# Kernel tuning notes

Measured on AMD Instinct MI355X. Metric: run time of the kernel, lower is better.

## Reference

```python
import jax, jax.numpy as jnp
import numpy as np

B, T, C, H = 4, 2048, 1024, 16
HD = C // H  # head_size = 64
EPS = 1e-5


def setup_inputs() -> dict:
    key = jax.random.key(0)
    ks = jax.random.split(key, 16)
    s_c = 1.0 / np.sqrt(C)
    s_4c = 1.0 / np.sqrt(4 * C)
    return {
        "x": jax.random.normal(ks[0], (B, T, C), jnp.float32),
        # per-head projections, stored [H, C, HD] (already in x@W orientation)
        "wq": jax.random.uniform(ks[1], (H, C, HD), jnp.float32, -s_c, s_c),
        "wk": jax.random.uniform(ks[2], (H, C, HD), jnp.float32, -s_c, s_c),
        "wv": jax.random.uniform(ks[3], (H, C, HD), jnp.float32, -s_c, s_c),
        "w_proj": jax.random.uniform(ks[4], (C, C), jnp.float32, -s_c, s_c),
        "b_proj": jax.random.uniform(ks[5], (C,), jnp.float32, -s_c, s_c),
        "w1": jax.random.uniform(ks[6], (C, 4 * C), jnp.float32, -s_c, s_c),
        "b1": jax.random.uniform(ks[7], (4 * C,), jnp.float32, -s_c, s_c),
        "w2": jax.random.uniform(ks[8], (4 * C, C), jnp.float32, -s_4c, s_4c),
        "b2": jax.random.uniform(ks[9], (C,), jnp.float32, -s_4c, s_4c),
        "ln1_g": jnp.ones((C,), jnp.float32),
        "ln1_b": jnp.zeros((C,), jnp.float32),
        "ln2_g": jnp.ones((C,), jnp.float32),
        "ln2_b": jnp.zeros((C,), jnp.float32),
    }


def layer_norm(x, g, b):
    mu = jnp.mean(x, axis=-1, keepdims=True)
    var = jnp.mean(jnp.square(x - mu), axis=-1, keepdims=True)
    return (x - mu) * jax.lax.rsqrt(var + EPS) * g + b


def reference(x, wq, wk, wv, w_proj, b_proj, w1, b1, w2, b2, ln1_g, ln1_b, ln2_g, ln2_b):
    Bc, Tc, Cc = x.shape
    h = layer_norm(x, ln1_g, ln1_b)
    q = jnp.einsum("btc,hcd->bhtd", h, wq)
    k = jnp.einsum("btc,hcd->bhtd", h, wk)
    v = jnp.einsum("btc,hcd->bhtd", h, wv)
    scale = HD ** -0.5
    wei = jnp.einsum("bhtd,bhsd->bhts", q, k) * scale  # [B,H,T,T]
    causal = jnp.tril(jnp.ones((Tc, Tc), bool))
    wei = jnp.where(causal, wei, -jnp.inf)
    wei = jax.nn.softmax(wei, axis=-1)
    att = jnp.einsum("bhts,bhsd->bhtd", wei, v)
    att = att.transpose(0, 2, 1, 3).reshape(Bc, Tc, Cc)  # concat heads
    x = x + att @ w_proj + b_proj
    h2 = layer_norm(x, ln2_g, ln2_b)
    ff = jax.nn.relu(h2 @ w1 + b1) @ w2 + b2
    return x + ff
```

## Files before the change

kernel.cpp:

```cpp
#include <hip/hip_runtime.h>


#define B_ 4
#define T_ 2048
#define C_ 1024
#define H_ 16
#define BT_ 8192

typedef __attribute__((ext_vector_type(8))) __bf16 bf16x8;
typedef __attribute__((ext_vector_type(4))) __bf16 bf16x4;
typedef __attribute__((ext_vector_type(4))) float f32x4;

#define WAIT_LGKM0 asm volatile("s_waitcnt lgkmcnt(0)" ::: "memory")
#define WAIT_VM(N) asm volatile("s_waitcnt vmcnt(" #N ")" ::: "memory")

__device__ __forceinline__ void gload_lds16(const void* g, void* l) {
  __builtin_amdgcn_global_load_lds((const __attribute__((address_space(1))) void*)g,
                                   (__attribute__((address_space(3))) void*)l, 16, 0, 0);
}

__device__ __forceinline__ void block_sync() {
  asm volatile("" ::: "memory");
  __builtin_amdgcn_s_barrier();
  asm volatile("" ::: "memory");
}

__global__ __launch_bounds__(256) void transpose_f32_bf16(
    const float* __restrict__ in, __bf16* __restrict__ out,
    int R, int Cc, long inBatch, long outBatch) {
  __shared__ float tile[32][33];
  const int tx = threadIdx.x, ty = threadIdx.y;
  in += (long)blockIdx.z * inBatch;
  out += (long)blockIdx.z * outBatch;
  const int r0 = blockIdx.y * 32, c0 = blockIdx.x * 32;
#pragma unroll
  for (int i = 0; i < 4; i++)
    tile[ty + i * 8][tx] = in[(long)(r0 + ty + i * 8) * Cc + c0 + tx];
  __syncthreads();
#pragma unroll
  for (int i = 0; i < 4; i++)
    out[(long)(c0 + ty + i * 8) * R + r0 + tx] = (__bf16)tile[tx][ty + i * 8];
}

__global__ __launch_bounds__(256) void ln_fwd(const float* __restrict__ x,
                                              const float* __restrict__ g,
                                              const float* __restrict__ bta,
                                              __bf16* __restrict__ out) {
  const long row = blockIdx.x;
  const int tid = threadIdx.x;
  float4 v = ((const float4*)(x + row * C_))[tid];
  float vals[4] = {v.x, v.y, v.z, v.w};
  float s = vals[0] + vals[1] + vals[2] + vals[3];
  float s2 = vals[0] * vals[0] + vals[1] * vals[1] + vals[2] * vals[2] + vals[3] * vals[3];
#pragma unroll
  for (int o = 1; o < 64; o <<= 1) {
    s += __shfl_xor(s, o);
    s2 += __shfl_xor(s2, o);
  }
  __shared__ float red[8];
  const int lane = tid & 63, wid = tid >> 6;
  if (lane == 0) { red[wid] = s; red[wid + 4] = s2; }
  __syncthreads();
  const float S = red[0] + red[1] + red[2] + red[3];
  const float S2 = red[4] + red[5] + red[6] + red[7];
  const float mu = S * (1.0f / C_);
  const float var = S2 * (1.0f / C_) - mu * mu;
  const float rs = rsqrtf(var + 1e-5f);
  bf16x4 o4;
#pragma unroll
  for (int j = 0; j < 4; j++) {
    const int c = tid * 4 + j;
    o4[j] = (__bf16)((vals[j] - mu) * rs * g[c] + bta[c]);
  }
  *(bf16x4*)(out + row * C_ + tid * 4) = o4;
}

template <int EPI>
__global__ __launch_bounds__(512, 2) void gemm8p(
    const __bf16* __restrict__ A, const __bf16* __restrict__ Bt,
    void* out0, void* out1, void* out2,
    const float* __restrict__ bias, const float* __restrict__ resid,
    int M, int N, int K, int nwg) {
  __shared__ __bf16 sm[49152];
  __bf16* ldsA = &sm[0];
  __bf16* ldsB = &sm[16384];
  const int tid = threadIdx.x, lane = tid & 63, wid = tid >> 6;
  const int wm = wid >> 2, wn = wid & 3;
  const int l15 = lane & 15, qtr = lane >> 4;
  const int q8 = nwg >> 3;
  const int wg = (blockIdx.x & 7) * q8 + (blockIdx.x >> 3);
  const int mBlocks = M >> 7;
  const long mBase = (long)(wg % mBlocks) * 128;
  const long nBase = (long)(wg / mBlocks) * 256;
  const int NT = K >> 6;

  f32x4 acc[4][4] = {};

  const int spos = (tid & 3) ^ ((tid >> 3) & 3);
  const __bf16* aS = A + (mBase + (tid >> 2)) * (long)K + spos * 8;
  const __bf16* bS0 = Bt + (nBase + (tid >> 2)) * (long)K + spos * 8;
  const __bf16* bS1 = bS0 + 128 * (long)K;

  const int posRd = (qtr ^ ((l15 >> 1) & 3)) * 8;
  const int aRd = (wm * 64 + l15) * 32 + posRd;
  const int bRd = (wn * 64 + l15) * 32 + posRd;

#define STG_A(BUF, KT, KH) gload_lds16(aS + (KT) * 64 + (KH) * 32, ldsA + (BUF) * 8192 + (KH) * 4096 + tid * 8)
#define STG_B(BUF, KT, KH)                                                                    \
  do {                                                                                        \
    gload_lds16(bS0 + (KT) * 64 + (KH) * 32, ldsB + (BUF) * 16384 + (KH) * 8192 + tid * 8);   \
    gload_lds16(bS1 + (KT) * 64 + (KH) * 32, ldsB + (BUF) * 16384 + (KH) * 8192 + 4096 + tid * 8); \
  } while (0)

#define GPHASE(BUF, KH, VMN, ...)                                                          \
  do {                                                                                     \
    bf16x8 af0 = *(const bf16x8*)&ldsA[(BUF) * 8192 + (KH) * 4096 + aRd];                  \
    bf16x8 af1 = *(const bf16x8*)&ldsA[(BUF) * 8192 + (KH) * 4096 + aRd + 512];            \
    bf16x8 af2 = *(const bf16x8*)&ldsA[(BUF) * 8192 + (KH) * 4096 + aRd + 1024];           \
    bf16x8 af3 = *(const bf16x8*)&ldsA[(BUF) * 8192 + (KH) * 4096 + aRd + 1536];           \
    bf16x8 bf0 = *(const bf16x8*)&ldsB[(BUF) * 16384 + (KH) * 8192 + bRd];                 \
    bf16x8 bf1 = *(const bf16x8*)&ldsB[(BUF) * 16384 + (KH) * 8192 + bRd + 512];           \
    bf16x8 bf2 = *(const bf16x8*)&ldsB[(BUF) * 16384 + (KH) * 8192 + bRd + 1024];          \
    bf16x8 bf3 = *(const bf16x8*)&ldsB[(BUF) * 16384 + (KH) * 8192 + bRd + 1536];          \
    __VA_ARGS__;                                                                           \
    WAIT_VM(VMN);                                                                          \
    block_sync();                                                                          \
    WAIT_LGKM0;                                                                            \
    __builtin_amdgcn_sched_barrier(0);                                                     \
    __builtin_amdgcn_s_setprio(1);                                                         \
    acc[0][0] = __builtin_amdgcn_mfma_f32_16x16x32_bf16(af0, bf0, acc[0][0], 0, 0, 0);     \
    acc[0][1] = __builtin_amdgcn_mfma_f32_16x16x32_bf16(af0, bf1, acc[0][1], 0, 0, 0);     \
    acc[0][2] = __builtin_amdgcn_mfma_f32_16x16x32_bf16(af0, bf2, acc[0][2], 0, 0, 0);     \
    acc[0][3] = __builtin_amdgcn_mfma_f32_16x16x32_bf16(af0, bf3, acc[0][3], 0, 0, 0);     \
    acc[1][0] = __builtin_amdgcn_mfma_f32_16x16x32_bf16(af1, bf0, acc[1][0], 0, 0, 0);     \
    acc[1][1] = __builtin_amdgcn_mfma_f32_16x16x32_bf16(af1, bf1, acc[1][1], 0, 0, 0);     \
    acc[1][2] = __builtin_amdgcn_mfma_f32_16x16x32_bf16(af1, bf2, acc[1][2], 0, 0, 0);     \
    acc[1][3] = __builtin_amdgcn_mfma_f32_16x16x32_bf16(af1, bf3, acc[1][3], 0, 0, 0);     \
    acc[2][0] = __builtin_amdgcn_mfma_f32_16x16x32_bf16(af2, bf0, acc[2][0], 0, 0, 0);     \
    acc[2][1] = __builtin_amdgcn_mfma_f32_16x16x32_bf16(af2, bf1, acc[2][1], 0, 0, 0);     \
    acc[2][2] = __builtin_amdgcn_mfma_f32_16x16x32_bf16(af2, bf2, acc[2][2], 0, 0, 0);     \
    acc[2][3] = __builtin_amdgcn_mfma_f32_16x16x32_bf16(af2, bf3, acc[2][3], 0, 0, 0);     \
    acc[3][0] = __builtin_amdgcn_mfma_f32_16x16x32_bf16(af3, bf0, acc[3][0], 0, 0, 0);     \
    acc[3][1] = __builtin_amdgcn_mfma_f32_16x16x32_bf16(af3, bf1, acc[3][1], 0, 0, 0);     \
    acc[3][2] = __builtin_amdgcn_mfma_f32_16x16x32_bf16(af3, bf2, acc[3][2], 0, 0, 0);     \
    acc[3][3] = __builtin_amdgcn_mfma_f32_16x16x32_bf16(af3, bf3, acc[3][3], 0, 0, 0);     \
    __builtin_amdgcn_s_setprio(0);                                                         \
    block_sync();                                                                          \
  } while (0)

  STG_A(0, 0, 0); STG_B(0, 0, 0);
  STG_A(0, 0, 1); STG_B(0, 0, 1);
  STG_A(1, 1, 0); STG_B(1, 1, 0);
  WAIT_VM(6);
  block_sync();

  for (int T = 0; T + 3 < NT; T += 2) {
    GPHASE(0, 0, 6, STG_A(1, T + 1, 1); STG_B(1, T + 1, 1));
    GPHASE(0, 1, 6, STG_A(0, T + 2, 0); STG_B(0, T + 2, 0));
    GPHASE(1, 0, 6, STG_A(0, T + 2, 1); STG_B(0, T + 2, 1));
    GPHASE(1, 1, 6, STG_A(1, T + 3, 0); STG_B(1, T + 3, 0));
  }
  GPHASE(0, 0, 6, STG_A(1, NT - 1, 1); STG_B(1, NT - 1, 1));
  GPHASE(0, 1, 3, );
  GPHASE(1, 0, 0, );
  GPHASE(1, 1, 0, );

#undef GPHASE
#undef STG_A
#undef STG_B

  if (EPI == 0) {
    __bf16* outB = (__bf16*)out0;
#pragma unroll
    for (int cf = 0; cf < 4; cf++) {
      const long gc = nBase + wn * 64 + cf * 16 + l15;
      const float bv = bias[gc];
#pragma unroll
      for (int rf = 0; rf < 4; rf++) {
        const long gr0 = mBase + wm * 64 + rf * 16 + qtr * 4;
#pragma unroll
        for (int r = 0; r < 4; r++)
          outB[(gr0 + r) * (long)N + gc] = (__bf16)fmaxf(acc[rf][cf][r] + bv, 0.0f);
      }
    }
  } else if (EPI == 2) {
    float* outF = (float*)out0;
#pragma unroll
    for (int cf = 0; cf < 4; cf++) {
      const long gc = nBase + wn * 64 + cf * 16 + l15;
      const float bv = bias[gc];
#pragma unroll
      for (int rf = 0; rf < 4; rf++) {
        const long gr0 = mBase + wm * 64 + rf * 16 + qtr * 4;
#pragma unroll
        for (int r = 0; r < 4; r++)
          outF[(gr0 + r) * (long)N + gc] = acc[rf][cf][r] + bv + resid[(gr0 + r) * (long)N + gc];
      }
    }
  } else {
    const int seg = (int)(nBase >> 10);
#pragma unroll
    for (int cf = 0; cf < 4; cf++) {
      const long gc = nBase + wn * 64 + cf * 16 + l15;
      const long cc = gc & 1023;
#pragma unroll
      for (int rf = 0; rf < 4; rf++) {
        const long gr0 = mBase + wm * 64 + rf * 16 + qtr * 4;
        if (seg == 0) {
          __bf16* Qb = (__bf16*)out0;
#pragma unroll
          for (int r = 0; r < 4; r++) Qb[(gr0 + r) * 1024 + cc] = (__bf16)acc[rf][cf][r];
        } else if (seg == 1) {
          __bf16* Kb = (__bf16*)out1;
#pragma unroll
          for (int r = 0; r < 4; r++) Kb[(gr0 + r) * 1024 + cc] = (__bf16)acc[rf][cf][r];
        } else {
          __bf16* Vtg = (__bf16*)out2;
          bf16x4 v4;
#pragma unroll
          for (int r = 0; r < 4; r++) v4[r] = (__bf16)acc[rf][cf][r];
          *(bf16x4*)&Vtg[cc * (long)BT_ + gr0] = v4;
        }
      }
    }
  }
}

#define PSTR 72
__global__ __launch_bounds__(512, 6) void attn_fwd2(
    const __bf16* __restrict__ Qg, const __bf16* __restrict__ Kg,
    const __bf16* __restrict__ Vtg, __bf16* __restrict__ O) {
  __shared__ __bf16 Ks[2][64 * 64];
  __shared__ __bf16 Vs[2][64 * 64];
  __shared__ __bf16 Ps[128 * PSTR];
  const int tid = threadIdx.x, lane = tid & 63, wid = tid >> 6;
  const int bh = blockIdx.x, b = bh >> 4, h = bh & 15;
  const int qx = 15 - blockIdx.y;
  const int qBase = qx * 128;
  const int qw = qBase + wid * 16;
  const int qwTop = qw + 15;
  const long bT = (long)b * T_;
  const int l15 = lane & 15, qtr = lane >> 4;
  const int q_lane = qw + l15;

  const int srow = tid >> 3;
  const int schunk = (tid & 7) ^ (srow & 7);
  const __bf16* kSrcBase = Kg + (bT + srow) * C_ + h * 64 + schunk * 8;
  const __bf16* vSrcBase = Vtg + (long)(h * 64 + srow) * BT_ + bT + schunk * 8;
  __bf16* kDst = &Ks[0][tid * 8];
  __bf16* vDst = &Vs[0][tid * 8];
  const int bufStride = 64 * 64;

  bf16x8 q0s, q1s;
  {
    const float SC = 0.125f * 1.44269504089f;
    bf16x8 r0 = *(const bf16x8*)(Qg + (bT + q_lane) * C_ + h * 64 + qtr * 8);
    bf16x8 r1 = *(const bf16x8*)(Qg + (bT + q_lane) * C_ + h * 64 + 32 + qtr * 8);
#pragma unroll
    for (int j = 0; j < 8; j++) {
      q0s[j] = (__bf16)((float)r0[j] * SC);
      q1s[j] = (__bf16)((float)r1[j] * SC);
    }
  }

  f32x4 o[4] = {};
  float m_ = -1e30f, l_ = 0.0f;
  const int nkt = 2 * qx + 2;

  gload_lds16(kSrcBase, kDst);
  gload_lds16(vSrcBase, vDst);
  __syncthreads();

  int buf = 0;
  for (int t = 0; t < nkt; t++) {
    const int k0 = t * 64;
    if (t + 1 < nkt) {
      const long koff = (long)(k0 + 64);
      gload_lds16(kSrcBase + koff * C_, kDst + (buf ^ 1) * bufStride);
      gload_lds16(vSrcBase + koff, vDst + (buf ^ 1) * bufStride);
    }
    if (k0 <= qwTop) {
      const __bf16* ks = Ks[buf];
      const __bf16* vs = Vs[buf];
      f32x4 sT[4] = {};
      __builtin_amdgcn_s_setprio(1);
#pragma unroll
      for (int kb = 0; kb < 4; kb++) {
        bf16x8 aK0 = *(const bf16x8*)&ks[(kb * 16 + l15) * 64 + ((qtr ^ (l15 & 7)) * 8)];
        bf16x8 aK1 = *(const bf16x8*)&ks[(kb * 16 + l15) * 64 + (((4 + qtr) ^ (l15 & 7)) * 8)];
        sT[kb] = __builtin_amdgcn_mfma_f32_16x16x32_bf16(aK0, q0s, sT[kb], 0, 0, 0);
        sT[kb] = __builtin_amdgcn_mfma_f32_16x16x32_bf16(aK1, q1s, sT[kb], 0, 0, 0);
      }
      __builtin_amdgcn_s_setprio(0);
      if (k0 + 63 > qw) {
#pragma unroll
        for (int kb = 0; kb < 4; kb++)
#pragma unroll
          for (int r = 0; r < 4; r++)
            if (k0 + kb * 16 + qtr * 4 + r > q_lane) sT[kb][r] = -1e30f;
      }
      float mx = -1e30f;
#pragma unroll
      for (int kb = 0; kb < 4; kb++)
#pragma unroll
        for (int r = 0; r < 4; r++) mx = fmaxf(mx, sT[kb][r]);
      mx = fmaxf(mx, __shfl_xor(mx, 16));
      mx = fmaxf(mx, __shfl_xor(mx, 32));
      const bool defer = __all(mx - m_ <= 8.0f);
      const float mnew = defer ? m_ : fmaxf(m_, mx);
      float psum = 0.0f;
#pragma unroll
      for (int kb = 0; kb < 4; kb++)
#pragma unroll
        for (int r = 0; r < 4; r++) {
          const float pv = exp2f(sT[kb][r] - mnew);
          psum += pv;
          Ps[(wid * 16 + l15) * PSTR + kb * 16 + qtr * 4 + r] = (__bf16)pv;
        }
      psum += __shfl_xor(psum, 16);
      psum += __shfl_xor(psum, 32);
      if (defer) {
        l_ += psum;
      } else {
        const float fac = exp2f(m_ - mnew);
        l_ = l_ * fac + psum;
        m_ = mnew;
#pragma unroll
        for (int r = 0; r < 4; r++) {
          const float fr = __shfl(fac, (lane & 48) + qtr * 4 + r);
#pragma unroll
          for (int dg = 0; dg < 4; dg++) o[dg][r] *= fr;
        }
      }
      __builtin_amdgcn_s_setprio(1);
#pragma unroll
      for (int s = 0; s < 2; s++) {
        bf16x8 aP = *(const bf16x8*)&Ps[(wid * 16 + l15) * PSTR + s * 32 + qtr * 8];
#pragma unroll
        for (int dg = 0; dg < 4; dg++) {
          bf16x8 bV = *(const bf16x8*)&vs[(dg * 16 + l15) * 64 + (((s * 4 + qtr) ^ (l15 & 7)) * 8)];
          o[dg] = __builtin_amdgcn_mfma_f32_16x16x32_bf16(aP, bV, o[dg], 0, 0, 0);
        }
      }
      __builtin_amdgcn_s_setprio(0);
    }
    __syncthreads();
    buf ^= 1;
  }

  const float linv = 1.0f / l_;
#pragma unroll
  for (int r = 0; r < 4; r++) {
    const float lr = __shfl(linv, (lane & 48) + qtr * 4 + r);
    const long row = bT + qw + qtr * 4 + r;
#pragma unroll
    for (int dg = 0; dg < 4; dg++)
      O[row * C_ + h * 64 + dg * 16 + l15] = (__bf16)(o[dg][r] * lr);
  }
}

extern "C" void kernel_launch(void* const* d_in, const int* in_sizes, int n_in,
                              void* d_out, int out_size, void* d_ws, size_t ws_size,
                              hipStream_t stream) {
  const float* x = (const float*)d_in[0];
  const float* wq = (const float*)d_in[1];
  const float* wk = (const float*)d_in[2];
  const float* wv = (const float*)d_in[3];
  const float* wproj = (const float*)d_in[4];
  const float* bproj = (const float*)d_in[5];
  const float* w1 = (const float*)d_in[6];
  const float* b1 = (const float*)d_in[7];
  const float* w2 = (const float*)d_in[8];
  const float* b2 = (const float*)d_in[9];
  const float* g1 = (const float*)d_in[10];
  const float* be1 = (const float*)d_in[11];
  const float* g2 = (const float*)d_in[12];
  const float* be2 = (const float*)d_in[13];

  char* ws = (char*)d_ws;
  const size_t MB = 1024ull * 1024ull;
  __bf16* h1 = (__bf16*)(ws + 0);
  __bf16* Qb = (__bf16*)(ws + 16 * MB);
  __bf16* Kb = (__bf16*)(ws + 32 * MB);
  __bf16* Vtg = (__bf16*)(ws + 48 * MB);
  __bf16* ff1 = (__bf16*)(ws + 32 * MB);
  __bf16* wqt = (__bf16*)(ws + 96 * MB);
  __bf16* wkt = (__bf16*)(ws + 98 * MB);
  __bf16* wvt = (__bf16*)(ws + 100 * MB);
  __bf16* wpt = (__bf16*)(ws + 102 * MB);
  __bf16* w1t = (__bf16*)(ws + 104 * MB);
  __bf16* w2t = (__bf16*)(ws + 112 * MB);
  __bf16* att = h1;
  __bf16* h2 = Qb;
  float* xout = (float*)d_out;

  dim3 tb(32, 8);
  transpose_f32_bf16<<<dim3(2, 32, 16), tb, 0, stream>>>(wq, wqt, 1024, 64, 1024 * 64, 64 * 1024);
  transpose_f32_bf16<<<dim3(2, 32, 16), tb, 0, stream>>>(wk, wkt, 1024, 64, 1024 * 64, 64 * 1024);
  transpose_f32_bf16<<<dim3(2, 32, 16), tb, 0, stream>>>(wv, wvt, 1024, 64, 1024 * 64, 64 * 1024);
  transpose_f32_bf16<<<dim3(32, 32, 1), tb, 0, stream>>>(wproj, wpt, 1024, 1024, 0, 0);
  transpose_f32_bf16<<<dim3(128, 32, 1), tb, 0, stream>>>(w1, w1t, 1024, 4096, 0, 0);
  transpose_f32_bf16<<<dim3(32, 128, 1), tb, 0, stream>>>(w2, w2t, 4096, 1024, 0, 0);

  ln_fwd<<<8192, 256, 0, stream>>>(x, g1, be1, h1);
  gemm8p<1><<<768, 512, 0, stream>>>(h1, wqt, Qb, Kb, Vtg, nullptr, nullptr, 8192, 3072, 1024, 768);
  attn_fwd2<<<dim3(64, 16), 512, 0, stream>>>(Qb, Kb, Vtg, att);
  gemm8p<2><<<256, 512, 0, stream>>>(att, wpt, xout, nullptr, nullptr, bproj, x, 8192, 1024, 1024, 256);
  ln_fwd<<<8192, 256, 0, stream>>>(xout, g2, be2, h2);
  gemm8p<0><<<1024, 512, 0, stream>>>(h2, w1t, ff1, nullptr, nullptr, b1, nullptr, 8192, 4096, 1024, 1024);
  gemm8p<2><<<256, 512, 0, stream>>>(ff1, w2t, xout, nullptr, nullptr, b2, (const float*)xout, 8192, 1024, 4096, 256);
}
```

Before: 383.8 us.

## Use 256x256 GEMM tiles with B-fragment reuse and split-K atomics for FF2

The GEMM tile grows from 128x256 to 256x256 per workgroup, with each wave covering 128 rows. B fragments are loaded once per K-half and reused across two A row-halves, raising arithmetic intensity per LDS read. The final FF2 GEMM uses a 2-way split-K whose partial sums are added with atomics onto the residual already in the output, so it keeps enough workgroups. In exchange, LDS grows to 128KB per block, which likely caps occupancy at one block per CU. The projection GEMM now launches only 128 workgroups, and the atomic accumulation order is nondeterministic.

Result: slower. 436.6 us (+13.8%).

```diff
diff --git a/kernel.cpp b/kernel.cpp
--- a/kernel.cpp
+++ b/kernel.cpp
@@ -13,6 +13,7 @@
 
 #define WAIT_LGKM0 asm volatile("s_waitcnt lgkmcnt(0)" ::: "memory")
 #define WAIT_VM(N) asm volatile("s_waitcnt vmcnt(" #N ")" ::: "memory")
+#define NOSTG ((void)0)
 
 __device__ __forceinline__ void gload_lds16(const void* g, void* l) {
   __builtin_amdgcn_global_load_lds((const __attribute__((address_space(1))) void*)g,
@@ -75,99 +76,117 @@
   *(bf16x4*)(out + row * C_ + tid * 4) = o4;
 }
 
-template <int EPI>
-__global__ __launch_bounds__(512, 2) void gemm8p(
+template <int EPI, int SPLITK>
+__global__ __launch_bounds__(512, 2) void gemm2x(
     const __bf16* __restrict__ A, const __bf16* __restrict__ Bt,
     void* out0, void* out1, void* out2,
     const float* __restrict__ bias, const float* __restrict__ resid,
     int M, int N, int K, int nwg) {
-  __shared__ __bf16 sm[49152];
+  __shared__ __bf16 sm[65536];
   __bf16* ldsA = &sm[0];
-  __bf16* ldsB = &sm[16384];
+  __bf16* ldsB = &sm[32768];
   const int tid = threadIdx.x, lane = tid & 63, wid = tid >> 6;
   const int wm = wid >> 2, wn = wid & 3;
   const int l15 = lane & 15, qtr = lane >> 4;
   const int q8 = nwg >> 3;
-  const int wg = (blockIdx.x & 7) * q8 + (blockIdx.x >> 3);
-  const int mBlocks = M >> 7;
-  const long mBase = (long)(wg % mBlocks) * 128;
+  int wg = (blockIdx.x & 7) * q8 + (blockIdx.x >> 3);
+  int k0 = 0, KS = K;
+  if (SPLITK) { KS = K >> 1; k0 = (wg >> 7) * KS; wg &= 127; }
+  const int mBlocks = M >> 8;
+  const long mBase = (long)(wg % mBlocks) * 256;
   const long nBase = (long)(wg / mBlocks) * 256;
-  const int NT = K >> 6;
-
-  f32x4 acc[4][4] = {};
+  const int NT = KS >> 6;
+
+  f32x4 acc[8][4] = {};
+  bf16x8 bfr[4];
+
+  const int posRd = (qtr ^ ((l15 >> 1) & 3)) * 8;
+  const int aRdB = (wm * 128 + l15) * 32 + posRd;
+  const int bRdB = (wn * 64 + l15) * 32 + posRd;
 
   const int spos = (tid & 3) ^ ((tid >> 3) & 3);
-  const __bf16* aS = A + (mBase + (tid >> 2)) * (long)K + spos * 8;
-  const __bf16* bS0 = Bt + (nBase + (tid >> 2)) * (long)K + spos * 8;
+  const __bf16* aS0 = A + (mBase + (tid >> 2)) * (long)K + k0 + spos * 8;
+  const __bf16* aS1 = aS0 + 128 * (long)K;
+  const __bf16* bS0 = Bt + (nBase + (tid >> 2)) * (long)K + k0 + spos * 8;
   const __bf16* bS1 = bS0 + 128 * (long)K;
 
-  const int posRd = (qtr ^ ((l15 >> 1) & 3)) * 8;
-  const int aRd = (wm * 64 + l15) * 32 + posRd;
-  const int bRd = (wn * 64 + l15) * 32 + posRd;
-
-#define STG_A(BUF, KT, KH) gload_lds16(aS + (KT) * 64 + (KH) * 32, ldsA + (BUF) * 8192 + (KH) * 4096 + tid * 8)
-#define STG_B(BUF, KT, KH)                                                                    \
+#define STGA(BUF, KH, KT)                                                                     \
   do {                                                                                        \
-    gload_lds16(bS0 + (KT) * 64 + (KH) * 32, ldsB + (BUF) * 16384 + (KH) * 8192 + tid * 8);   \
-    gload_lds16(bS1 + (KT) * 64 + (KH) * 32, ldsB + (BUF) * 16384 + (KH) * 8192 + 4096 + tid * 8); \
+    gload_lds16(aS0 + (KT) * 64 + (KH) * 32, ldsA + ((BUF) * 2 + (KH)) * 8192 + tid * 8);     \
+    gload_lds16(aS1 + (KT) * 64 + (KH) * 32, ldsA + ((BUF) * 2 + (KH)) * 8192 + 4096 + tid * 8); \
   } while (0)
-
-#define GPHASE(BUF, KH, VMN, ...)                                                          \
-  do {                                                                                     \
-    bf16x8 af0 = *(const bf16x8*)&ldsA[(BUF) * 8192 + (KH) * 4096 + aRd];                  \
-    bf16x8 af1 = *(const bf16x8*)&ldsA[(BUF) * 8192 + (KH) * 4096 + aRd + 512];            \
-    bf16x8 af2 = *(const bf16x8*)&ldsA[(BUF) * 8192 + (KH) * 4096 + aRd + 1024];           \
-    bf16x8 af3 = *(const bf16x8*)&ldsA[(BUF) * 8192 + (KH) * 4096 + aRd + 1536];           \
-    bf16x8 bf0 = *(const bf16x8*)&ldsB[(BUF) * 16384 + (KH) * 8192 + bRd];                 \
-    bf16x8 bf1 = *(const bf16x8*)&ldsB[(BUF) * 16384 + (KH) * 8192 + bRd + 512];           \
-    bf16x8 bf2 = *(const bf16x8*)&ldsB[(BUF) * 16384 + (KH) * 8192 + bRd + 1024];          \
-    bf16x8 bf3 = *(const bf16x8*)&ldsB[(BUF) * 16384 + (KH) * 8192 + bRd + 1536];          \
-    __VA_ARGS__;                                                                           \
-    WAIT_VM(VMN);                                                                          \
-    block_sync();                                                                          \
-    WAIT_LGKM0;                                                                            \
-    __builtin_amdgcn_sched_barrier(0);                                                     \
-    __builtin_amdgcn_s_setprio(1);                                                         \
-    acc[0][0] = __builtin_amdgcn_mfma_f32_16x16x32_bf16(af0, bf0, acc[0][0], 0, 0, 0);     \
-    acc[0][1] = __builtin_amdgcn_mfma_f32_16x16x32_bf16(af0, bf1, acc[0][1], 0, 0, 0);     \
-    acc[0][2] = __builtin_amdgcn_mfma_f32_16x16x32_bf16(af0, bf2, acc[0][2], 0, 0, 0);     \
-    acc[0][3] = __builtin_amdgcn_mfma_f32_16x16x32_bf16(af0, bf3, acc[0][3], 0, 0, 0);     \
-    acc[1][0] = __builtin_amdgcn_mfma_f32_16x16x32_bf16(af1, bf0, acc[1][0], 0, 0, 0);     \
-    acc[1][1] = __builtin_amdgcn_mfma_f32_16x16x32_bf16(af1, bf1, acc[1][1], 0, 0, 0);     \
-    acc[1][2] = __builtin_amdgcn_mfma_f32_16x16x32_bf16(af1, bf2, acc[1][2], 0, 0, 0);     \
-    acc[1][3] = __builtin_amdgcn_mfma_f32_16x16x32_bf16(af1, bf3, acc[1][3], 0, 0, 0);     \
-    acc[2][0] = __builtin_amdgcn_mfma_f32_16x16x32_bf16(af2, bf0, acc[2][0], 0, 0, 0);     \
-    acc[2][1] = __builtin_amdgcn_mfma_f32_16x16x32_bf16(af2, bf1, acc[2][1], 0, 0, 0);     \
-    acc[2][2] = __builtin_amdgcn_mfma_f32_16x16x32_bf16(af2, bf2, acc[2][2], 0, 0, 0);     \
-    acc[2][3] = __builtin_amdgcn_mfma_f32_16x16x32_bf16(af2, bf3, acc[2][3], 0, 0, 0);     \
-    acc[3][0] = __builtin_amdgcn_mfma_f32_16x16x32_bf16(af3, bf0, acc[3][0], 0, 0, 0);     \
-    acc[3][1] = __builtin_amdgcn_mfma_f32_16x16x32_bf16(af3, bf1, acc[3][1], 0, 0, 0);     \
-    acc[3][2] = __builtin_amdgcn_mfma_f32_16x16x32_bf16(af3, bf2, acc[3][2], 0, 0, 0);     \
-    acc[3][3] = __builtin_amdgcn_mfma_f32_16x16x32_bf16(af3, bf3, acc[3][3], 0, 0, 0);     \
-    __builtin_amdgcn_s_setprio(0);                                                         \
-    block_sync();                                                                          \
+#define STGB(BUF, KH, KT)                                                                     \
+  do {                                                                                        \
+    gload_lds16(bS0 + (KT) * 64 + (KH) * 32, ldsB + ((BUF) * 2 + (KH)) * 8192 + tid * 8);     \
+    gload_lds16(bS1 + (KT) * 64 + (KH) * 32, ldsB + ((BUF) * 2 + (KH)) * 8192 + 4096 + tid * 8); \
   } while (0)
 
-  STG_A(0, 0, 0); STG_B(0, 0, 0);
-  STG_A(0, 0, 1); STG_B(0, 0, 1);
-  STG_A(1, 1, 0); STG_B(1, 1, 0);
-  WAIT_VM(6);
+#define PH(BUF, KH, RFH, WAITOP, STG)                                                        \
+  do {                                                                                       \
+    const __bf16* sA_ = ldsA + ((BUF) * 2 + (KH)) * 8192;                                    \
+    const __bf16* sB_ = ldsB + ((BUF) * 2 + (KH)) * 8192;                                    \
+    bf16x8 af0 = *(const bf16x8*)&sA_[aRdB + (RFH) * 2048];                                  \
+    bf16x8 af1 = *(const bf16x8*)&sA_[aRdB + (RFH) * 2048 + 512];                            \
+    bf16x8 af2 = *(const bf16x8*)&sA_[aRdB + (RFH) * 2048 + 1024];                           \
+    bf16x8 af3 = *(const bf16x8*)&sA_[aRdB + (RFH) * 2048 + 1536];                           \
+    if ((RFH) == 0) {                                                                        \
+      bfr[0] = *(const bf16x8*)&sB_[bRdB];                                                   \
+      bfr[1] = *(const bf16x8*)&sB_[bRdB + 512];                                             \
+      bfr[2] = *(const bf16x8*)&sB_[bRdB + 1024];                                            \
+      bfr[3] = *(const bf16x8*)&sB_[bRdB + 1536];                                            \
+    }                                                                                        \
+    STG;                                                                                     \
+    WAITOP;                                                                                  \
+    block_sync();                                                                            \
+    WAIT_LGKM0;                                                                              \
+    __builtin_amdgcn_sched_barrier(0);                                                       \
+    __builtin_amdgcn_s_setprio(1);                                                           \
+    acc[(RFH)*4+0][0] = __builtin_amdgcn_mfma_f32_16x16x32_bf16(af0, bfr[0], acc[(RFH)*4+0][0], 0, 0, 0); \
+    acc[(RFH)*4+0][1] = __builtin_amdgcn_mfma_f32_16x16x32_bf16(af0, bfr[1], acc[(RFH)*4+0][1], 0, 0, 0); \
+    acc[(RFH)*4+0][2] = __builtin_amdgcn_mfma_f32_16x16x32_bf16(af0, bfr[2], acc[(RFH)*4+0][2], 0, 0, 0); \
+    acc[(RFH)*4+0][3] = __builtin_amdgcn_mfma_f32_16x16x32_bf16(af0, bfr[3], acc[(RFH)*4+0][3], 0, 0, 0); \
+    acc[(RFH)*4+1][0] = __builtin_amdgcn_mfma_f32_16x16x32_bf16(af1, bfr[0], acc[(RFH)*4+1][0], 0, 0, 0); \
+    acc[(RFH)*4+1][1] = __builtin_amdgcn_mfma_f32_16x16x32_bf16(af1, bfr[1], acc[(RFH)*4+1][1], 0, 0, 0); \
+    acc[(RFH)*4+1][2] = __builtin_amdgcn_mfma_f32_16x16x32_bf16(af1, bfr[2], acc[(RFH)*4+1][2], 0, 0, 0); \
+    acc[(RFH)*4+1][3] = __builtin_amdgcn_mfma_f32_16x16x32_bf16(af1, bfr[3], acc[(RFH)*4+1][3], 0, 0, 0); \
+    acc[(RFH)*4+2][0] = __builtin_amdgcn_mfma_f32_16x16x32_bf16(af2, bfr[0], acc[(RFH)*4+2][0], 0, 0, 0); \
+    acc[(RFH)*4+2][1] = __builtin_amdgcn_mfma_f32_16x16x32_bf16(af2, bfr[1], acc[(RFH)*4+2][1], 0, 0, 0); \
+    acc[(RFH)*4+2][2] = __builtin_amdgcn_mfma_f32_16x16x32_bf16(af2, bfr[2], acc[(RFH)*4+2][2], 0, 0, 0); \
+    acc[(RFH)*4+2][3] = __builtin_amdgcn_mfma_f32_16x16x32_bf16(af2, bfr[3], acc[(RFH)*4+2][3], 0, 0, 0); \
+    acc[(RFH)*4+3][0] = __builtin_amdgcn_mfma_f32_16x16x32_bf16(af3, bfr[0], acc[(RFH)*4+3][0], 0, 0, 0); \
+    acc[(RFH)*4+3][1] = __builtin_amdgcn_mfma_f32_16x16x32_bf16(af3, bfr[1], acc[(RFH)*4+3][1], 0, 0, 0); \
+    acc[(RFH)*4+3][2] = __builtin_amdgcn_mfma_f32_16x16x32_bf16(af3, bfr[2], acc[(RFH)*4+3][2], 0, 0, 0); \
+    acc[(RFH)*4+3][3] = __builtin_amdgcn_mfma_f32_16x16x32_bf16(af3, bfr[3], acc[(RFH)*4+3][3], 0, 0, 0); \
+    __builtin_amdgcn_s_setprio(0);                                                           \
+    block_sync();                                                                            \
+  } while (0)
+
+  STGA(0, 0, 0); STGB(0, 0, 0);
+  STGA(0, 1, 0); STGB(0, 1, 0);
+  STGA(1, 0, 1); STGB(1, 0, 1);
+  WAIT_VM(8);
   block_sync();
 
-  for (int T = 0; T + 3 < NT; T += 2) {
-    GPHASE(0, 0, 6, STG_A(1, T + 1, 1); STG_B(1, T + 1, 1));
-    GPHASE(0, 1, 6, STG_A(0, T + 2, 0); STG_B(0, T + 2, 0));
-    GPHASE(1, 0, 6, STG_A(0, T + 2, 1); STG_B(0, T + 2, 1));
-    GPHASE(1, 1, 6, STG_A(1, T + 3, 0); STG_B(1, T + 3, 0));
-  }
-  GPHASE(0, 0, 6, STG_A(1, NT - 1, 1); STG_B(1, NT - 1, 1));
-  GPHASE(0, 1, 3, );
-  GPHASE(1, 0, 0, );
-  GPHASE(1, 1, 0, );
-
-#undef GPHASE
-#undef STG_A
-#undef STG_B
+  int b = 0;
+  for (int t = 0; t + 2 < NT; ++t) {
+    PH(b, 0, 0, NOSTG, STGA(b ^ 1, 1, t + 1));
+    PH(b, 0, 1, WAIT_VM(8), STGB(b ^ 1, 1, t + 1));
+    PH(b, 1, 0, NOSTG, STGA(b, 0, t + 2));
+    PH(b, 1, 1, WAIT_VM(8), STGB(b, 0, t + 2));
+    b ^= 1;
+  }
+  PH(0, 0, 0, NOSTG, STGA(1, 1, NT - 1));
+  PH(0, 0, 1, WAIT_VM(8), STGB(1, 1, NT - 1));
+  PH(0, 1, 0, NOSTG, NOSTG);
+  PH(0, 1, 1, WAIT_VM(4), NOSTG);
+  PH(1, 0, 0, NOSTG, NOSTG);
+  PH(1, 0, 1, WAIT_VM(0), NOSTG);
+  PH(1, 1, 0, NOSTG, NOSTG);
+  PH(1, 1, 1, WAIT_VM(0), NOSTG);
+
+#undef PH
+#undef STGA
+#undef STGB
 
   if (EPI == 0) {
     __bf16* outB = (__bf16*)out0;
@@ -176,8 +195,8 @@
       const long gc = nBase + wn * 64 + cf * 16 + l15;
       const float bv = bias[gc];
 #pragma unroll
-      for (int rf = 0; rf < 4; rf++) {
-        const long gr0 = mBase + wm * 64 + rf * 16 + qtr * 4;
+      for (int rf = 0; rf < 8; rf++) {
+        const long gr0 = mBase + wm * 128 + rf * 16 + qtr * 4;
 #pragma unroll
         for (int r = 0; r < 4; r++)
           outB[(gr0 + r) * (long)N + gc] = (__bf16)fmaxf(acc[rf][cf][r] + bv, 0.0f);
@@ -190,11 +209,25 @@
       const long gc = nBase + wn * 64 + cf * 16 + l15;
       const float bv = bias[gc];
 #pragma unroll
-      for (int rf = 0; rf < 4; rf++) {
-        const long gr0 = mBase + wm * 64 + rf * 16 + qtr * 4;
+      for (int rf = 0; rf < 8; rf++) {
+        const long gr0 = mBase + wm * 128 + rf * 16 + qtr * 4;
 #pragma unroll
         for (int r = 0; r < 4; r++)
           outF[(gr0 + r) * (long)N + gc] = acc[rf][cf][r] + bv + resid[(gr0 + r) * (long)N + gc];
+      }
+    }
+  } else if (EPI == 3) {
+    float* outF = (float*)out0;
+#pragma unroll
+    for (int cf = 0; cf < 4; cf++) {
+      const long gc = nBase + wn * 64 + cf * 16 + l15;
+      const float bv = (k0 == 0) ? bias[gc] : 0.0f;
+#pragma unroll
+      for (int rf = 0; rf < 8; rf++) {
+        const long gr0 = mBase + wm * 128 + rf * 16 + qtr * 4;
+#pragma unroll
+        for (int r = 0; r < 4; r++)
+          atomicAdd(&outF[(gr0 + r) * (long)N + gc], acc[rf][cf][r] + bv);
       }
     }
   } else {
@@ -204,8 +237,8 @@
       const long gc = nBase + wn * 64 + cf * 16 + l15;
       const long cc = gc & 1023;
 #pragma unroll
-      for (int rf = 0; rf < 4; rf++) {
-        const long gr0 = mBase + wm * 64 + rf * 16 + qtr * 4;
+      for (int rf = 0; rf < 8; rf++) {
+        const long gr0 = mBase + wm * 128 + rf * 16 + qtr * 4;
         if (seg == 0) {
           __bf16* Qb = (__bf16*)out0;
 #pragma unroll
@@ -403,10 +436,10 @@
   transpose_f32_bf16<<<dim3(32, 128, 1), tb, 0, stream>>>(w2, w2t, 4096, 1024, 0, 0);
 
   ln_fwd<<<8192, 256, 0, stream>>>(x, g1, be1, h1);
-  gemm8p<1><<<768, 512, 0, stream>>>(h1, wqt, Qb, Kb, Vtg, nullptr, nullptr, 8192, 3072, 1024, 768);
+  gemm2x<1, 0><<<384, 512, 0, stream>>>(h1, wqt, Qb, Kb, Vtg, nullptr, nullptr, 8192, 3072, 1024, 384);
   attn_fwd2<<<dim3(64, 16), 512, 0, stream>>>(Qb, Kb, Vtg, att);
-  gemm8p<2><<<256, 512, 0, stream>>>(att, wpt, xout, nullptr, nullptr, bproj, x, 8192, 1024, 1024, 256);
+  gemm2x<2, 0><<<128, 512, 0, stream>>>(att, wpt, xout, nullptr, nullptr, bproj, x, 8192, 1024, 1024, 128);
   ln_fwd<<<8192, 256, 0, stream>>>(xout, g2, be2, h2);
-  gemm8p<0><<<1024, 512, 0, stream>>>(h2, w1t, ff1, nullptr, nullptr, b1, nullptr, 8192, 4096, 1024, 1024);
-  gemm8p<2><<<256, 512, 0, stream>>>(ff1, w2t, xout, nullptr, nullptr, b2, (const float*)xout, 8192, 1024, 4096, 256);
-}
+  gemm2x<0, 0><<<512, 512, 0, stream>>>(h2, w1t, ff1, nullptr, nullptr, b1, nullptr, 8192, 4096, 1024, 512);
+  gemm2x<3, 1><<<256, 512, 0, stream>>>(ff1, w2t, xout, nullptr, nullptr, b2, nullptr, 8192, 1024, 4096, 256);
+}
```

## Process 32 query rows per wave in attention to reuse K/V tiles

Applied to the files above, without the earlier changes.

The attention kernel now gives each wave two 16-row query sub-tiles (256 queries per block, 8 blocks per head instead of 16). Each K and V fragment read from LDS therefore feeds twice as many MFMAs, and the per-block K/V global loads are amortized over more queries. P tiles are written to LDS as packed 4-element vectors instead of scalars. The cost is more registers (launch bounds lowered from 6 to 4 waves/SIMD), a larger P buffer, fewer blocks for load balance, and more wasted work on causal-diagonal tiles.

Measured after the change: 393.2 us. 2.4% more time.

```diff
diff --git a/kernel.cpp b/kernel.cpp
--- a/kernel.cpp
+++ b/kernel.cpp
@@ -227,21 +227,19 @@
 }
 
 #define PSTR 72
-__global__ __launch_bounds__(512, 6) void attn_fwd2(
+__global__ __launch_bounds__(512, 4) void attn_fwd3(
     const __bf16* __restrict__ Qg, const __bf16* __restrict__ Kg,
     const __bf16* __restrict__ Vtg, __bf16* __restrict__ O) {
   __shared__ __bf16 Ks[2][64 * 64];
   __shared__ __bf16 Vs[2][64 * 64];
-  __shared__ __bf16 Ps[128 * PSTR];
+  __shared__ __bf16 Ps[256 * PSTR];
   const int tid = threadIdx.x, lane = tid & 63, wid = tid >> 6;
   const int bh = blockIdx.x, b = bh >> 4, h = bh & 15;
-  const int qx = 15 - blockIdx.y;
-  const int qBase = qx * 128;
-  const int qw = qBase + wid * 16;
-  const int qwTop = qw + 15;
+  const int qx = 7 - blockIdx.y;
+  const int qB = qx * 256;
+  const int qw = qB + wid * 32;
   const long bT = (long)b * T_;
   const int l15 = lane & 15, qtr = lane >> 4;
-  const int q_lane = qw + l15;
 
   const int srow = tid >> 3;
   const int schunk = (tid & 7) ^ (srow & 7);
@@ -251,21 +249,29 @@
   __bf16* vDst = &Vs[0][tid * 8];
   const int bufStride = 64 * 64;
 
-  bf16x8 q0s, q1s;
+  __bf16* psW0 = &Ps[(wid * 32 + l15) * PSTR + qtr * 4];
+  __bf16* psW1 = psW0 + 16 * PSTR;
+  const __bf16* psR0 = &Ps[(wid * 32 + l15) * PSTR + qtr * 8];
+  const __bf16* psR1 = psR0 + 16 * PSTR;
+
+  bf16x8 q0s[2], q1s[2];
   {
     const float SC = 0.125f * 1.44269504089f;
-    bf16x8 r0 = *(const bf16x8*)(Qg + (bT + q_lane) * C_ + h * 64 + qtr * 8);
-    bf16x8 r1 = *(const bf16x8*)(Qg + (bT + q_lane) * C_ + h * 64 + 32 + qtr * 8);
-#pragma unroll
-    for (int j = 0; j < 8; j++) {
-      q0s[j] = (__bf16)((float)r0[j] * SC);
-      q1s[j] = (__bf16)((float)r1[j] * SC);
-    }
-  }
-
-  f32x4 o[4] = {};
-  float m_ = -1e30f, l_ = 0.0f;
-  const int nkt = 2 * qx + 2;
+#pragma unroll
+    for (int hf = 0; hf < 2; hf++) {
+      bf16x8 r0 = *(const bf16x8*)(Qg + (bT + qw + l15) * C_ + h * 64 + hf * 32 + qtr * 8);
+      bf16x8 r1 = *(const bf16x8*)(Qg + (bT + qw + 16 + l15) * C_ + h * 64 + hf * 32 + qtr * 8);
+#pragma unroll
+      for (int j = 0; j < 8; j++) {
+        q0s[hf][j] = (__bf16)((float)r0[j] * SC);
+        q1s[hf][j] = (__bf16)((float)r1[j] * SC);
+      }
+    }
+  }
+
+  f32x4 o0[4] = {}, o1[4] = {};
+  float m0 = -1e30f, m1 = -1e30f, l0 = 0.0f, l1 = 0.0f;
+  const int nkt = 4 * qx + 4;
 
   gload_lds16(kSrcBase, kDst);
   gload_lds16(vSrcBase, vDst);
@@ -279,67 +285,86 @@
       gload_lds16(kSrcBase + koff * C_, kDst + (buf ^ 1) * bufStride);
       gload_lds16(vSrcBase + koff, vDst + (buf ^ 1) * bufStride);
     }
-    if (k0 <= qwTop) {
+    if (k0 <= qw + 31) {
       const __bf16* ks = Ks[buf];
       const __bf16* vs = Vs[buf];
-      f32x4 sT[4] = {};
+      f32x4 sT0[4] = {}, sT1[4] = {};
       __builtin_amdgcn_s_setprio(1);
 #pragma unroll
       for (int kb = 0; kb < 4; kb++) {
         bf16x8 aK0 = *(const bf16x8*)&ks[(kb * 16 + l15) * 64 + ((qtr ^ (l15 & 7)) * 8)];
         bf16x8 aK1 = *(const bf16x8*)&ks[(kb * 16 + l15) * 64 + (((4 + qtr) ^ (l15 & 7)) * 8)];
-        sT[kb] = __builtin_amdgcn_mfma_f32_16x16x32_bf16(aK0, q0s, sT[kb], 0, 0, 0);
-        sT[kb] = __builtin_amdgcn_mfma_f32_16x16x32_bf16(aK1, q1s, sT[kb], 0, 0, 0);
+        sT0[kb] = __builtin_amdgcn_mfma_f32_16x16x32_bf16(aK0, q0s[0], sT0[kb], 0, 0, 0);
+        sT0[kb] = __builtin_amdgcn_mfma_f32_16x16x32_bf16(aK1, q0s[1], sT0[kb], 0, 0, 0);
+        sT1[kb] = __builtin_amdgcn_mfma_f32_16x16x32_bf16(aK0, q1s[0], sT1[kb], 0, 0, 0);
+        sT1[kb] = __builtin_amdgcn_mfma_f32_16x16x32_bf16(aK1, q1s[1], sT1[kb], 0, 0, 0);
       }
       __builtin_amdgcn_s_setprio(0);
       if (k0 + 63 > qw) {
 #pragma unroll
         for (int kb = 0; kb < 4; kb++)
 #pragma unroll
-          for (int r = 0; r < 4; r++)
-            if (k0 + kb * 16 + qtr * 4 + r > q_lane) sT[kb][r] = -1e30f;
-      }
-      float mx = -1e30f;
+          for (int r = 0; r < 4; r++) {
+            const int kk = k0 + kb * 16 + qtr * 4 + r;
+            if (kk > qw + l15) sT0[kb][r] = -1e30f;
+            if (kk > qw + 16 + l15) sT1[kb][r] = -1e30f;
+          }
+      }
+      float mx0 = -1e30f, mx1 = -1e30f;
 #pragma unroll
       for (int kb = 0; kb < 4; kb++)
 #pragma unroll
-        for (int r = 0; r < 4; r++) mx = fmaxf(mx, sT[kb][r]);
-      mx = fmaxf(mx, __shfl_xor(mx, 16));
-      mx = fmaxf(mx, __shfl_xor(mx, 32));
-      const bool defer = __all(mx - m_ <= 8.0f);
-      const float mnew = defer ? m_ : fmaxf(m_, mx);
-      float psum = 0.0f;
-#pragma unroll
-      for (int kb = 0; kb < 4; kb++)
-#pragma unroll
         for (int r = 0; r < 4; r++) {
-          const float pv = exp2f(sT[kb][r] - mnew);
-          psum += pv;
-          Ps[(wid * 16 + l15) * PSTR + kb * 16 + qtr * 4 + r] = (__bf16)pv;
+          mx0 = fmaxf(mx0, sT0[kb][r]);
+          mx1 = fmaxf(mx1, sT1[kb][r]);
         }
-      psum += __shfl_xor(psum, 16);
-      psum += __shfl_xor(psum, 32);
+      mx0 = fmaxf(mx0, __shfl_xor(mx0, 16));
+      mx0 = fmaxf(mx0, __shfl_xor(mx0, 32));
+      mx1 = fmaxf(mx1, __shfl_xor(mx1, 16));
+      mx1 = fmaxf(mx1, __shfl_xor(mx1, 32));
+      const bool defer = __all(mx0 - m0 <= 8.0f && mx1 - m1 <= 8.0f);
+      const float mn0 = defer ? m0 : fmaxf(m0, mx0);
+      const float mn1 = defer ? m1 : fmaxf(m1, mx1);
+      float ps0 = 0.0f, ps1 = 0.0f;
+#pragma unroll
+      for (int kb = 0; kb < 4; kb++) {
+        bf16x4 p4a, p4b;
+#pragma unroll
+        for (int r = 0; r < 4; r++) {
+          const float pa = exp2f(sT0[kb][r] - mn0);
+          const float pb = exp2f(sT1[kb][r] - mn1);
+          ps0 += pa; ps1 += pb;
+          p4a[r] = (__bf16)pa; p4b[r] = (__bf16)pb;
+        }
+        *(bf16x4*)&psW0[kb * 16] = p4a;
+        *(bf16x4*)&psW1[kb * 16] = p4b;
+      }
+      ps0 += __shfl_xor(ps0, 16); ps0 += __shfl_xor(ps0, 32);
+      ps1 += __shfl_xor(ps1, 16); ps1 += __shfl_xor(ps1, 32);
       if (defer) {
-        l_ += psum;
+        l0 += ps0; l1 += ps1;
       } else {
-        const float fac = exp2f(m_ - mnew);
-        l_ = l_ * fac + psum;
-        m_ = mnew;
+        const float f0 = exp2f(m0 - mn0), f1 = exp2f(m1 - mn1);
+        l0 = l0 * f0 + ps0; l1 = l1 * f1 + ps1;
+        m0 = mn0; m1 = mn1;
 #pragma unroll
         for (int r = 0; r < 4; r++) {
-          const float fr = __shfl(fac, (lane & 48) + qtr * 4 + r);
-#pragma unroll
-          for (int dg = 0; dg < 4; dg++) o[dg][r] *= fr;
+          const float fr0 = __shfl(f0, (lane & 48) + qtr * 4 + r);
+          const float fr1 = __shfl(f1, (lane & 48) + qtr * 4 + r);
+#pragma unroll
+          for (int dg = 0; dg < 4; dg++) { o0[dg][r] *= fr0; o1[dg][r] *= fr1; }
         }
       }
       __builtin_amdgcn_s_setprio(1);
 #pragma unroll
       for (int s = 0; s < 2; s++) {
-        bf16x8 aP = *(const bf16x8*)&Ps[(wid * 16 + l15) * PSTR + s * 32 + qtr * 8];
+        bf16x8 aP0 = *(const bf16x8*)&psR0[s * 32];
+        bf16x8 aP1 = *(const bf16x8*)&psR1[s * 32];
 #pragma unroll
         for (int dg = 0; dg < 4; dg++) {
           bf16x8 bV = *(const bf16x8*)&vs[(dg * 16 + l15) * 64 + (((s * 4 + qtr) ^ (l15 & 7)) * 8)];
-          o[dg] = __builtin_amdgcn_mfma_f32_16x16x32_bf16(aP, bV, o[dg], 0, 0, 0);
+          o0[dg] = __builtin_amdgcn_mfma_f32_16x16x32_bf16(aP0, bV, o0[dg], 0, 0, 0);
+          o1[dg] = __builtin_amdgcn_mfma_f32_16x16x32_bf16(aP1, bV, o1[dg], 0, 0, 0);
         }
       }
       __builtin_amdgcn_s_setprio(0);
@@ -348,14 +373,17 @@
     buf ^= 1;
   }
 
-  const float linv = 1.0f / l_;
+  const float li0 = 1.0f / l0, li1 = 1.0f / l1;
 #pragma unroll
   for (int r = 0; r < 4; r++) {
-    const float lr = __shfl(linv, (lane & 48) + qtr * 4 + r);
-    const long row = bT + qw + qtr * 4 + r;
-#pragma unroll
-    for (int dg = 0; dg < 4; dg++)
-      O[row * C_ + h * 64 + dg * 16 + l15] = (__bf16)(o[dg][r] * lr);
+    const float lr0 = __shfl(li0, (lane & 48) + qtr * 4 + r);
+    const float lr1 = __shfl(li1, (lane & 48) + qtr * 4 + r);
+    const long row0 = bT + qw + qtr * 4 + r;
+#pragma unroll
+    for (int dg = 0; dg < 4; dg++) {
+      O[row0 * C_ + h * 64 + dg * 16 + l15] = (__bf16)(o0[dg][r] * lr0);
+      O[(row0 + 16) * C_ + h * 64 + dg * 16 + l15] = (__bf16)(o1[dg][r] * lr1);
+    }
   }
 }
 
@@ -404,7 +432,7 @@
 
   ln_fwd<<<8192, 256, 0, stream>>>(x, g1, be1, h1);
   gemm8p<1><<<768, 512, 0, stream>>>(h1, wqt, Qb, Kb, Vtg, nullptr, nullptr, 8192, 3072, 1024, 768);
-  attn_fwd2<<<dim3(64, 16), 512, 0, stream>>>(Qb, Kb, Vtg, att);
+  attn_fwd3<<<dim3(64, 8), 512, 0, stream>>>(Qb, Kb, Vtg, att);
   gemm8p<2><<<256, 512, 0, stream>>>(att, wpt, xout, nullptr, nullptr, bproj, x, 8192, 1024, 1024, 256);
   ln_fwd<<<8192, 256, 0, stream>>>(xout, g2, be2, h2);
   gemm8p<0><<<1024, 512, 0, stream>>>(h2, w1t, ff1, nullptr, nullptr, b1, nullptr, 8192, 4096, 1024, 1024);
```
